# Optimization experiments

Measured on AMD Instinct MI355X. Metric: run time of the kernel, lower is better.

The kernel has to match this reference:

```python
import jax, jax.numpy as jnp
import numpy as np

QLEN, BSZ, D_MODEL = 2048, 2, 1024
N_HEAD, D_HEAD = 16, 64
SCALE = 1.0 / (D_HEAD ** 0.5)
LN_EPS = 1e-5


def _rel_shift(x):
    # x: [qlen, klen, bsz, n_head]
    q, k, b, n = x.shape
    zero_pad = jnp.zeros((q, 1, b, n), dtype=x.dtype)
    x_padded = jnp.concatenate([zero_pad, x], axis=1).reshape(k + 1, q, b, n)
    return x_padded[1:].reshape(q, k, b, n)


def setup_inputs() -> dict:
    key = jax.random.key(0)
    ks = jax.random.split(key, 6)
    w = jax.random.normal(ks[0], (QLEN, BSZ, D_MODEL), dtype=jnp.float32)
    r_emb = jax.random.normal(ks[1], (QLEN, N_HEAD, D_HEAD), dtype=jnp.float32) * 0.02
    r_w_bias = jax.random.normal(ks[2], (N_HEAD, D_HEAD), dtype=jnp.float32) * 0.02
    r_bias = jax.random.normal(ks[3], (QLEN, N_HEAD), dtype=jnp.float32) * 0.02
    # causal mask (1 above diagonal => masked), dim==2 branch of original forward
    attn_mask = jnp.triu(jnp.ones((QLEN, QLEN), dtype=jnp.float32), k=1)
    W_qkv = jax.random.normal(ks[4], (D_MODEL, 3 * N_HEAD * D_HEAD), dtype=jnp.float32) * (D_MODEL ** -0.5)
    W_o = jax.random.normal(ks[5], (N_HEAD * D_HEAD, D_MODEL), dtype=jnp.float32) * (D_MODEL ** -0.5)
    ln_g = jnp.ones((D_MODEL,), dtype=jnp.float32)
    ln_b = jnp.zeros((D_MODEL,), dtype=jnp.float32)
    return {"w": w, "r_emb": r_emb, "r_w_bias": r_w_bias, "r_bias": r_bias,
            "attn_mask": attn_mask, "W_qkv": W_qkv, "W_o": W_o, "ln_g": ln_g, "ln_b": ln_b}


def reference(w, r_emb, r_w_bias, r_bias, attn_mask, W_qkv, W_o, ln_g, ln_b):
    qlen, bsz, d_model = w.shape
    n_head, d_head = r_w_bias.shape

    w_heads = w @ W_qkv                                   # [q, b, 3*n*d]
    q_h, k_h, v_h = jnp.split(w_heads, 3, axis=-1)
    q_h = q_h.reshape(qlen, bsz, n_head, d_head)
    k_h = k_h.reshape(qlen, bsz, n_head, d_head)
    v_h = v_h.reshape(qlen, bsz, n_head, d_head)
    klen = k_h.shape[0]

    # klen == r_emb.size(0) here, so slicing is a no-op (kept for fidelity)
    r_emb_s = r_emb[-klen:]
    r_bias_s = r_bias[-klen:]

    rw_head_q = q_h + r_w_bias[None, None]                # [q, b, n, d]
    AC = jnp.einsum('ibnd,jbnd->ijbn', rw_head_q, k_h)    # content-content
    B_ = jnp.einsum('ibnd,jnd->ijbn', q_h, r_emb_s)       # content-position
    D_ = r_bias_s[None, :, None, :]                       # [1, k, 1, n]
    BD = _rel_shift(B_ + D_)

    attn_score = (AC + BD) * SCALE
    attn_score = attn_score + attn_mask[:, :, None, None] * (-1e9)
    attn_prob = jax.nn.softmax(attn_score, axis=1)

    attn_vec = jnp.einsum('ijbn,jbnd->ibnd', attn_prob, v_h)
    attn_vec = attn_vec.reshape(qlen, bsz, n_head * d_head)
    attn_out = attn_vec @ W_o

    # residual + LayerNorm
    y = w + attn_out
    mu = jnp.mean(y, axis=-1, keepdims=True)
    var = jnp.var(y, axis=-1, keepdims=True)
    return (y - mu) / jnp.sqrt(var + LN_EPS) * ln_g + ln_b
```

## Files before the change

kernel.cpp:

```cpp
#include <hip/hip_runtime.h>

typedef unsigned short ushort_t;
typedef unsigned short us4 __attribute__((ext_vector_type(4)));
typedef unsigned short us8 __attribute__((ext_vector_type(8)));
typedef unsigned int   u32x4 __attribute__((ext_vector_type(4)));
typedef float          f32x4 __attribute__((ext_vector_type(4)));
typedef __bf16         bf16x8 __attribute__((ext_vector_type(8)));

__device__ __forceinline__ unsigned short f2bf(float f) {
  unsigned u = __builtin_bit_cast(unsigned, f);
  u += 0x7fffu + ((u >> 16) & 1u);
  return (unsigned short)(u >> 16);
}
__device__ __forceinline__ float bf2f(unsigned short h) {
  unsigned u = ((unsigned)h) << 16;
  return __builtin_bit_cast(float, u);
}


__global__ __launch_bounds__(256) void k_conv_x(const float* __restrict__ in,
                                                ushort_t* __restrict__ out) {
  int i = (blockIdx.x * 256 + threadIdx.x) * 4;
  float4 v = *(const float4*)(in + i);
  us4 o;
  o[0] = f2bf(v.x); o[1] = f2bf(v.y); o[2] = f2bf(v.z); o[3] = f2bf(v.w);
  *(us4*)(out + i) = o;
}

__global__ __launch_bounds__(256) void k_transpose_bf16(const float* __restrict__ in,
                                                        ushort_t* __restrict__ out,
                                                        int R, int C) {
  __shared__ float tile[32][33];
  int c0 = blockIdx.x * 32, r0 = blockIdx.y * 32;
  int tx = threadIdx.x, ty = threadIdx.y;
#pragma unroll
  for (int k = 0; k < 32; k += 8)
    tile[ty + k][tx] = in[(size_t)(r0 + ty + k) * C + c0 + tx];
  __syncthreads();
#pragma unroll
  for (int k = 0; k < 32; k += 8)
    out[(size_t)(c0 + ty + k) * R + r0 + tx] = f2bf(tile[tx][ty + k]);
}

__global__ __launch_bounds__(256) void k_conv_remb(const float* __restrict__ re,
                                                   ushort_t* __restrict__ out) {
  int tid = blockIdx.x * 256 + threadIdx.x;
  int o = tid * 8;
  int d = o & 63, r = (o >> 6) & 2047, h = o >> 17;
  const float* src = re + ((size_t)r * 16 + h) * 64 + d;
  float4 a = *(const float4*)(src);
  float4 b = *(const float4*)(src + 4);
  us8 u;
  u[0] = f2bf(a.x); u[1] = f2bf(a.y); u[2] = f2bf(a.z); u[3] = f2bf(a.w);
  u[4] = f2bf(b.x); u[5] = f2bf(b.y); u[6] = f2bf(b.z); u[7] = f2bf(b.w);
  *(us8*)(out + o) = u;
}

__global__ __launch_bounds__(256) void k_rbias2(const ushort_t* __restrict__ RE,
                                                const float* __restrict__ rwb,
                                                const float* __restrict__ rbias,
                                                float* __restrict__ out) {
  int tid = blockIdx.x * 256 + threadIdx.x;
  int h = tid >> 11, r = tid & 2047;
  const ushort_t* re = RE + ((size_t)h * 2048 + r) * 64;
  const float* wv = rwb + h * 64;
  float acc = 0.f;
#pragma unroll
  for (int d0 = 0; d0 < 64; d0 += 8) {
    us8 v = *(const us8*)(re + d0);
#pragma unroll
    for (int e = 0; e < 8; ++e) acc += bf2f(v[e]) * wv[d0 + e];
  }
  out[h * 2048 + r] = (rbias[r * 16 + h] - acc) * 0.125f;
}


__global__ __launch_bounds__(256) void k_gemm_qkv(const ushort_t* __restrict__ A,
                                                  const ushort_t* __restrict__ B,
                                                  const float* __restrict__ rwb,
                                                  ushort_t* __restrict__ qt,
                                                  ushort_t* __restrict__ kk,
                                                  ushort_t* __restrict__ vv) {
  __shared__ ushort_t Al[128 * 32], Bl[128 * 32];
  int row0 = blockIdx.x * 128, col0 = blockIdx.y * 128;
  int t = threadIdx.x, w = t >> 6, l = t & 63;
  int wr = w >> 1, wc = w & 1, g = l >> 4, cl = l & 15;
  f32x4 acc[4][4];
#pragma unroll
  for (int m = 0; m < 4; ++m)
#pragma unroll
    for (int n = 0; n < 4; ++n) acc[m][n] = (f32x4){0.f, 0.f, 0.f, 0.f};
  for (int k0 = 0; k0 < 1024; k0 += 32) {
#pragma unroll
    for (int c = 0; c < 2; ++c) {
      int u = t + 256 * c, row = u >> 2, col = (u & 3) * 8;
      *(u32x4*)(&Al[row * 32 + col]) = *(const u32x4*)(A + (size_t)(row0 + row) * 1024 + k0 + col);
      *(u32x4*)(&Bl[row * 32 + col]) = *(const u32x4*)(B + (size_t)(col0 + row) * 1024 + k0 + col);
    }
    __syncthreads();
    bf16x8 af[4], bfr[4];
#pragma unroll
    for (int m = 0; m < 4; ++m) af[m] = *(const bf16x8*)(&Al[(wr * 64 + m * 16 + cl) * 32 + g * 8]);
#pragma unroll
    for (int n = 0; n < 4; ++n) bfr[n] = *(const bf16x8*)(&Bl[(wc * 64 + n * 16 + cl) * 32 + g * 8]);
#pragma unroll
    for (int m = 0; m < 4; ++m)
#pragma unroll
      for (int n = 0; n < 4; ++n)
        acc[m][n] = __builtin_amdgcn_mfma_f32_16x16x32_bf16(af[m], bfr[n], acc[m][n], 0, 0, 0);
    __syncthreads();
  }
  int sec = col0 >> 10;
#pragma unroll
  for (int m = 0; m < 4; ++m) {
#pragma unroll
    for (int n = 0; n < 4; ++n) {
#pragma unroll
      for (int r = 0; r < 4; ++r) {
        int row = row0 + wr * 64 + m * 16 + g * 4 + r;
        int col = col0 + wc * 64 + n * 16 + cl;
        int mm = col & 1023, hh = mm >> 6, d = mm & 63;
        int bq = row & 1, iq = row >> 1;
        float val = acc[m][n][r];
        if (sec == 0) {
          qt[(((size_t)bq * 16 + hh) * 2048 + iq) * 64 + d] = f2bf((val + rwb[mm]) * 0.125f);
        } else if (sec == 1) {
          kk[(((size_t)bq * 16 + hh) * 2048 + iq) * 64 + d] = f2bf(val);
        } else {
          vv[(((size_t)bq * 16 + hh) * 64 + d) * 2048 + iq] = f2bf(val);
        }
      }
    }
  }
}


__global__ __launch_bounds__(256, 3) void k_flash(const ushort_t* __restrict__ QT,
                                                  const ushort_t* __restrict__ KK,
                                                  const ushort_t* __restrict__ VT,
                                                  const ushort_t* __restrict__ RE,
                                                  const float* __restrict__ RB2,
                                                  ushort_t* __restrict__ AV) {
  int bh = blockIdx.x, b = bh >> 4, h = bh & 15;
  int i0 = (gridDim.y - 1 - blockIdx.y) * 64;
  int t = threadIdx.x, w = t >> 6, l = t & 63, g = l >> 4, cl = l & 15;

  __shared__ ushort_t Klds[64 * 72];
  __shared__ ushort_t Vt[64 * 72];
  __shared__ ushort_t Rl[128 * 72];
  __shared__ float rb2s[128];
  __shared__ ushort_t Pls[4][16 * 72];
  __shared__ float alphal[4][16];
  __shared__ float lsuml[4][16];

  const ushort_t* qb = QT + ((size_t)(b * 16 + h)) * 2048 * 64;
  const ushort_t* kb = KK + ((size_t)(b * 16 + h)) * 2048 * 64;
  const ushort_t* vt = VT + ((size_t)(b * 16 + h)) * 64 * 2048;
  const ushort_t* rbase = RE + (size_t)h * 2048 * 64;
  const float* r2 = RB2 + h * 2048;

  int qrow = i0 + w * 16 + cl;
  bf16x8 qa0 = *(const bf16x8*)(qb + (size_t)qrow * 64 + g * 8);
  bf16x8 qa1 = *(const bf16x8*)(qb + (size_t)qrow * 64 + 32 + g * 8);

  float m_run[4], l_run[4];
  f32x4 Ot[4];
#pragma unroll
  for (int r = 0; r < 4; ++r) { m_run[r] = -1e30f; l_run[r] = 0.f; }
#pragma unroll
  for (int dt = 0; dt < 4; ++dt) Ot[dt] = (f32x4){0.f, 0.f, 0.f, 0.f};

  int nt = gridDim.y - blockIdx.y;
  int rb0f = 1984 - i0;
  int urow = t >> 3, ucol = (t & 7) * 8;

  *(u32x4*)(&Rl[((rb0f + urow) & 127) * 72 + ucol]) =
      *(const u32x4*)(rbase + (size_t)(rb0f + urow) * 64 + ucol);
  *(u32x4*)(&Rl[((rb0f + urow + 32) & 127) * 72 + ucol]) =
      *(const u32x4*)(rbase + (size_t)(rb0f + urow + 32) * 64 + ucol);
  if (t < 64) rb2s[(rb0f + t) & 127] = r2[rb0f + t];

  u32x4 kreg0, kreg1, vreg0, vreg1, rreg0, rreg1;
  float rb2reg;

  {
    int j0n = 0;
    kreg0 = *(const u32x4*)(kb + (size_t)(j0n + urow) * 64 + ucol);
    kreg1 = *(const u32x4*)(kb + (size_t)(j0n + urow + 32) * 64 + ucol);
    vreg0 = *(const u32x4*)(vt + (size_t)urow * 2048 + j0n + ucol);
    vreg1 = *(const u32x4*)(vt + (size_t)(urow + 32) * 2048 + j0n + ucol);
    int gs = rb0f + 64;
    int rr0 = gs + urow, rr1 = gs + urow + 32;
    rreg0 = (rr0 < 2048) ? *(const u32x4*)(rbase + (size_t)rr0 * 64 + ucol) : (u32x4){0u, 0u, 0u, 0u};
    rreg1 = (rr1 < 2048) ? *(const u32x4*)(rbase + (size_t)rr1 * 64 + ucol) : (u32x4){0u, 0u, 0u, 0u};
    int rrb = gs + t;
    rb2reg = (t < 64 && rrb < 2048) ? r2[rrb] : 0.f;
  }

  for (int tt = 0; tt < nt; ++tt) {
    int j0 = tt * 64;
    int rb0 = rb0f + j0;
    __syncthreads();
    {
      *(u32x4*)(&Klds[urow * 72 + ucol]) = kreg0;
      *(u32x4*)(&Klds[(urow + 32) * 72 + ucol]) = kreg1;
      *(u32x4*)(&Vt[urow * 72 + ucol]) = vreg0;
      *(u32x4*)(&Vt[(urow + 32) * 72 + ucol]) = vreg1;
      int gs = rb0 + 64;
      *(u32x4*)(&Rl[((gs + urow) & 127) * 72 + ucol]) = rreg0;
      *(u32x4*)(&Rl[((gs + urow + 32) & 127) * 72 + ucol]) = rreg1;
      if (t < 64) rb2s[(gs + t) & 127] = rb2reg;
    }
    __syncthreads();
    if (tt + 1 < nt) {
      int j0n = j0 + 64;
      kreg0 = *(const u32x4*)(kb + (size_t)(j0n + urow) * 64 + ucol);
      kreg1 = *(const u32x4*)(kb + (size_t)(j0n + urow + 32) * 64 + ucol);
      vreg0 = *(const u32x4*)(vt + (size_t)urow * 2048 + j0n + ucol);
      vreg1 = *(const u32x4*)(vt + (size_t)(urow + 32) * 2048 + j0n + ucol);
      int gs = rb0f + j0n + 64;
      int rr0 = gs + urow, rr1 = gs + urow + 32;
      rreg0 = (rr0 < 2048) ? *(const u32x4*)(rbase + (size_t)rr0 * 64 + ucol) : (u32x4){0u, 0u, 0u, 0u};
      rreg1 = (rr1 < 2048) ? *(const u32x4*)(rbase + (size_t)rr1 * 64 + ucol) : (u32x4){0u, 0u, 0u, 0u};
      int rrb = gs + t;
      rb2reg = (t < 64 && rrb < 2048) ? r2[rrb] : 0.f;
    }

    int bw0 = 48 - 16 * w;
    int rB = rb0 + bw0;
    f32x4 bwf[5];
#pragma unroll
    for (int ct = 0; ct < 5; ++ct) {
      int prow = (rB + ct * 16) & 127;
      f32x4 a = (f32x4){0.f, 0.f, 0.f, 0.f};
      bf16x8 rr0 = *(const bf16x8*)(&Rl[(prow + cl) * 72 + g * 8]);
      a = __builtin_amdgcn_mfma_f32_16x16x32_bf16(qa0, rr0, a, 0, 0, 0);
      bf16x8 rr1 = *(const bf16x8*)(&Rl[(prow + cl) * 72 + 32 + g * 8]);
      a = __builtin_amdgcn_mfma_f32_16x16x32_bf16(qa1, rr1, a, 0, 0, 0);
      float rv = rb2s[(prow + cl) & 127];
      a[0] += rv; a[1] += rv; a[2] += rv; a[3] += rv;
      bwf[ct] = a;
    }

    f32x4 S[4];
#pragma unroll
    for (int ct = 0; ct < 4; ++ct) {
      f32x4 a = (f32x4){0.f, 0.f, 0.f, 0.f};
      bf16x8 kf0 = *(const bf16x8*)(&Klds[(ct * 16 + cl) * 72 + g * 8]);
      a = __builtin_amdgcn_mfma_f32_16x16x32_bf16(qa0, kf0, a, 0, 0, 0);
      bf16x8 kf1 = *(const bf16x8*)(&Klds[(ct * 16 + cl) * 72 + 32 + g * 8]);
      a = __builtin_amdgcn_mfma_f32_16x16x32_bf16(qa1, kf1, a, 0, 0, 0);
      S[ct] = a;
    }

    int climit = i0 - j0 + 15 + 16 * w;
#pragma unroll
    for (int r = 0; r < 4; ++r) {
      int rl = g * 4 + r;
      int dlt = cl - rl + 15;
      int src = (l & 48) | (dlt & 15);
      float b0 = __shfl(bwf[0][r], src);
      float b1 = __shfl(bwf[1][r], src);
      float b2 = __shfl(bwf[2][r], src);
      float b3 = __shfl(bwf[3][r], src);
      float b4 = __shfl(bwf[4][r], src);
      if (dlt >= 16) { b0 = b1; b1 = b2; b2 = b3; b3 = b4; }
      float sv[4];
      sv[0] = (dlt      <= climit) ? S[0][r] + b0 : -1e30f;
      sv[1] = (dlt + 16 <= climit) ? S[1][r] + b1 : -1e30f;
      sv[2] = (dlt + 32 <= climit) ? S[2][r] + b2 : -1e30f;
      sv[3] = (dlt + 48 <= climit) ? S[3][r] + b3 : -1e30f;
      float rmax = fmaxf(fmaxf(sv[0], sv[1]), fmaxf(sv[2], sv[3]));
      rmax = fmaxf(rmax, __shfl_xor(rmax, 1));
      rmax = fmaxf(rmax, __shfl_xor(rmax, 2));
      rmax = fmaxf(rmax, __shfl_xor(rmax, 4));
      rmax = fmaxf(rmax, __shfl_xor(rmax, 8));
      float mn = fmaxf(m_run[r], rmax);
      float al = __expf(m_run[r] - mn);
      m_run[r] = mn;
      float rsum = 0.f;
#pragma unroll
      for (int ct = 0; ct < 4; ++ct) {
        float pv = __expf(sv[ct] - mn);
        sv[ct] = pv;
        rsum += pv;
      }
      rsum += __shfl_xor(rsum, 1);
      rsum += __shfl_xor(rsum, 2);
      rsum += __shfl_xor(rsum, 4);
      rsum += __shfl_xor(rsum, 8);
      l_run[r] = l_run[r] * al + rsum;
      if (cl == 0) alphal[w][rl] = al;
#pragma unroll
      for (int ct = 0; ct < 4; ++ct)
        Pls[w][rl * 72 + ct * 16 + cl] = f2bf(sv[ct]);
    }
    __syncthreads();

    float aq = alphal[w][cl];
    bf16x8 pb0 = *(const bf16x8*)(&Pls[w][cl * 72 + g * 8]);
    bf16x8 pb1 = *(const bf16x8*)(&Pls[w][cl * 72 + 32 + g * 8]);
#pragma unroll
    for (int dt = 0; dt < 4; ++dt) {
      f32x4 o = Ot[dt];
      o[0] *= aq; o[1] *= aq; o[2] *= aq; o[3] *= aq;
      bf16x8 va0 = *(const bf16x8*)(&Vt[(dt * 16 + cl) * 72 + g * 8]);
      o = __builtin_amdgcn_mfma_f32_16x16x32_bf16(va0, pb0, o, 0, 0, 0);
      bf16x8 va1 = *(const bf16x8*)(&Vt[(dt * 16 + cl) * 72 + 32 + g * 8]);
      o = __builtin_amdgcn_mfma_f32_16x16x32_bf16(va1, pb1, o, 0, 0, 0);
      Ot[dt] = o;
    }
  }

  if (cl == 0) {
#pragma unroll
    for (int r = 0; r < 4; ++r) lsuml[w][g * 4 + r] = l_run[r];
  }
  float inv = 1.f / lsuml[w][cl];
  int orow = (i0 + w * 16 + cl) * 2 + b;
#pragma unroll
  for (int dt = 0; dt < 4; ++dt) {
    us4 o4;
    o4[0] = f2bf(Ot[dt][0] * inv);
    o4[1] = f2bf(Ot[dt][1] * inv);
    o4[2] = f2bf(Ot[dt][2] * inv);
    o4[3] = f2bf(Ot[dt][3] * inv);
    *(us4*)(&AV[(size_t)orow * 1024 + h * 64 + dt * 16 + g * 4]) = o4;
  }
}


__global__ __launch_bounds__(256) void k_gemm_o(const ushort_t* __restrict__ A,
                                                const ushort_t* __restrict__ B,
                                                const float* __restrict__ wsrc,
                                                float* __restrict__ Y) {
  __shared__ ushort_t Al[128 * 32], Bl[128 * 32];
  int row0 = blockIdx.x * 128, col0 = blockIdx.y * 128;
  int t = threadIdx.x, w = t >> 6, l = t & 63;
  int wr = w >> 1, wc = w & 1, g = l >> 4, cl = l & 15;
  f32x4 acc[4][4];
#pragma unroll
  for (int m = 0; m < 4; ++m)
#pragma unroll
    for (int n = 0; n < 4; ++n) acc[m][n] = (f32x4){0.f, 0.f, 0.f, 0.f};
  for (int k0 = 0; k0 < 1024; k0 += 32) {
#pragma unroll
    for (int c = 0; c < 2; ++c) {
      int u = t + 256 * c, row = u >> 2, col = (u & 3) * 8;
      *(u32x4*)(&Al[row * 32 + col]) = *(const u32x4*)(A + (size_t)(row0 + row) * 1024 + k0 + col);
      *(u32x4*)(&Bl[row * 32 + col]) = *(const u32x4*)(B + (size_t)(col0 + row) * 1024 + k0 + col);
    }
    __syncthreads();
    bf16x8 af[4], bfr[4];
#pragma unroll
    for (int m = 0; m < 4; ++m) af[m] = *(const bf16x8*)(&Al[(wr * 64 + m * 16 + cl) * 32 + g * 8]);
#pragma unroll
    for (int n = 0; n < 4; ++n) bfr[n] = *(const bf16x8*)(&Bl[(wc * 64 + n * 16 + cl) * 32 + g * 8]);
#pragma unroll
    for (int m = 0; m < 4; ++m)
#pragma unroll
      for (int n = 0; n < 4; ++n)
        acc[m][n] = __builtin_amdgcn_mfma_f32_16x16x32_bf16(af[m], bfr[n], acc[m][n], 0, 0, 0);
    __syncthreads();
  }
#pragma unroll
  for (int m = 0; m < 4; ++m) {
#pragma unroll
    for (int n = 0; n < 4; ++n) {
#pragma unroll
      for (int r = 0; r < 4; ++r) {
        int row = row0 + wr * 64 + m * 16 + g * 4 + r;
        int col = col0 + wc * 64 + n * 16 + cl;
        size_t idx = (size_t)row * 1024 + col;
        Y[idx] = acc[m][n][r] + wsrc[idx];
      }
    }
  }
}


__global__ __launch_bounds__(256) void k_ln(const float* __restrict__ Y,
                                            const float* __restrict__ gg,
                                            const float* __restrict__ bb,
                                            float* __restrict__ out) {
  int row = blockIdx.x, t = threadIdx.x;
  float4 v = *(const float4*)(Y + (size_t)row * 1024 + t * 4);
  float s = v.x + v.y + v.z + v.w;
  float q = v.x * v.x + v.y * v.y + v.z * v.z + v.w * v.w;
#pragma unroll
  for (int m = 32; m >= 1; m >>= 1) {
    s += __shfl_xor(s, m);
    q += __shfl_xor(q, m);
  }
  __shared__ float ssh[4], qsh[4];
  int w = t >> 6, l = t & 63;
  if (l == 0) { ssh[w] = s; qsh[w] = q; }
  __syncthreads();
  s = ssh[0] + ssh[1] + ssh[2] + ssh[3];
  q = qsh[0] + qsh[1] + qsh[2] + qsh[3];
  float mu = s * (1.f / 1024.f);
  float var = q * (1.f / 1024.f) - mu * mu;
  float rstd = rsqrtf(var + 1e-5f);
  float4 gv = *(const float4*)(gg + t * 4);
  float4 bv = *(const float4*)(bb + t * 4);
  float4 o;
  o.x = (v.x - mu) * rstd * gv.x + bv.x;
  o.y = (v.y - mu) * rstd * gv.y + bv.y;
  o.z = (v.z - mu) * rstd * gv.z + bv.z;
  o.w = (v.w - mu) * rstd * gv.w + bv.w;
  *(float4*)(out + (size_t)row * 1024 + t * 4) = o;
}


extern "C" void kernel_launch(void* const* d_in, const int* in_sizes, int n_in,
                              void* d_out, int out_size, void* d_ws, size_t ws_size,
                              hipStream_t stream) {
  const float* w      = (const float*)d_in[0];
  const float* r_emb  = (const float*)d_in[1];
  const float* r_w_b  = (const float*)d_in[2];
  const float* r_bias = (const float*)d_in[3];
  const float* W_qkv  = (const float*)d_in[5];
  const float* W_o    = (const float*)d_in[6];
  const float* ln_g   = (const float*)d_in[7];
  const float* ln_b   = (const float*)d_in[8];
  float* out = (float*)d_out;
  char* ws = (char*)d_ws;

  ushort_t* X16  = (ushort_t*)(ws + 0);
  ushort_t* WQ16 = (ushort_t*)(ws + 8388608);
  ushort_t* WO16 = (ushort_t*)(ws + 14680064);
  ushort_t* RE16 = (ushort_t*)(ws + 16777216);
  float*    RB2  = (float*)(ws + 20971520);
  ushort_t* QT16 = (ushort_t*)(ws + 21102592);
  ushort_t* K16  = (ushort_t*)(ws + 29491200);
  ushort_t* VT16 = (ushort_t*)(ws + 37879808);
  ushort_t* AV16 = (ushort_t*)(ws + 46268416);
  float*    Y32  = (float*)(ws + 54657024);

  k_conv_x<<<4096, 256, 0, stream>>>(w, X16);
  k_transpose_bf16<<<dim3(96, 32), dim3(32, 8), 0, stream>>>(W_qkv, WQ16, 1024, 3072);
  k_transpose_bf16<<<dim3(32, 32), dim3(32, 8), 0, stream>>>(W_o, WO16, 1024, 1024);
  k_conv_remb<<<1024, 256, 0, stream>>>(r_emb, RE16);
  k_rbias2<<<128, 256, 0, stream>>>(RE16, r_w_b, r_bias, RB2);
  k_gemm_qkv<<<dim3(32, 24), 256, 0, stream>>>(X16, WQ16, r_w_b, QT16, K16, VT16);
  k_flash<<<dim3(32, 32), 256, 0, stream>>>(QT16, K16, VT16, RE16, RB2, AV16);
  k_gemm_o<<<dim3(32, 8), 256, 0, stream>>>(AV16, WO16, w, Y32);
  k_ln<<<4096, 256, 0, stream>>>(Y32, ln_g, ln_b, out);
}
```

Before: 201.2 us.

## Enlarge flash query tile to 128 rows with 8 waves; async global-to-LDS loads in GEMMs

The flash attention kernel now handles 128 query rows per block with 512 threads (8 waves), so each K/V/R tile loaded into LDS is shared by twice as many query rows. The block count halves, and the relative-position ring buffer grows to 256 rows. Separately, both GEMMs stage A/B tiles with global_load_lds direct-to-LDS copies instead of loads through registers. The cost is more LDS per block and coarser causal-imbalance granularity. The async copies rely on the LDS layout staying contiguous, which holds because row*32+col equals u*8.

```diff
diff --git a/kernel.cpp b/kernel.cpp
--- a/kernel.cpp
+++ b/kernel.cpp
@@ -15,6 +15,12 @@
 __device__ __forceinline__ float bf2f(unsigned short h) {
   unsigned u = ((unsigned)h) << 16;
   return __builtin_bit_cast(float, u);
+}
+
+__device__ __forceinline__ void async_cp16(const ushort_t* g, ushort_t* l) {
+  __builtin_amdgcn_global_load_lds(
+      (const __attribute__((address_space(1))) unsigned int*)g,
+      (__attribute__((address_space(3))) unsigned int*)l, 16, 0, 0);
 }
 
 
@@ -94,8 +100,8 @@
 #pragma unroll
     for (int c = 0; c < 2; ++c) {
       int u = t + 256 * c, row = u >> 2, col = (u & 3) * 8;
-      *(u32x4*)(&Al[row * 32 + col]) = *(const u32x4*)(A + (size_t)(row0 + row) * 1024 + k0 + col);
-      *(u32x4*)(&Bl[row * 32 + col]) = *(const u32x4*)(B + (size_t)(col0 + row) * 1024 + k0 + col);
+      async_cp16(A + (size_t)(row0 + row) * 1024 + k0 + col, &Al[u * 8]);
+      async_cp16(B + (size_t)(col0 + row) * 1024 + k0 + col, &Bl[u * 8]);
     }
     __syncthreads();
     bf16x8 af[4], bfr[4];
@@ -135,23 +141,24 @@
 }
 
 
-__global__ __launch_bounds__(256, 3) void k_flash(const ushort_t* __restrict__ QT,
+__global__ __launch_bounds__(512, 4) void k_flash(const ushort_t* __restrict__ QT,
                                                   const ushort_t* __restrict__ KK,
                                                   const ushort_t* __restrict__ VT,
                                                   const ushort_t* __restrict__ RE,
                                                   const float* __restrict__ RB2,
                                                   ushort_t* __restrict__ AV) {
   int bh = blockIdx.x, b = bh >> 4, h = bh & 15;
-  int i0 = (gridDim.y - 1 - blockIdx.y) * 64;
+  int i0 = (gridDim.y - 1 - blockIdx.y) * 128;
   int t = threadIdx.x, w = t >> 6, l = t & 63, g = l >> 4, cl = l & 15;
+  int ib = i0 + 16 * w;
 
   __shared__ ushort_t Klds[64 * 72];
   __shared__ ushort_t Vt[64 * 72];
-  __shared__ ushort_t Rl[128 * 72];
-  __shared__ float rb2s[128];
-  __shared__ ushort_t Pls[4][16 * 72];
-  __shared__ float alphal[4][16];
-  __shared__ float lsuml[4][16];
+  __shared__ ushort_t Rl[256 * 72];
+  __shared__ float rb2s[256];
+  __shared__ ushort_t Pls[8][16 * 72];
+  __shared__ float alphal[8][16];
+  __shared__ float lsuml[8][16];
 
   const ushort_t* qb = QT + ((size_t)(b * 16 + h)) * 2048 * 64;
   const ushort_t* kb = KK + ((size_t)(b * 16 + h)) * 2048 * 64;
@@ -159,7 +166,7 @@
   const ushort_t* rbase = RE + (size_t)h * 2048 * 64;
   const float* r2 = RB2 + h * 2048;
 
-  int qrow = i0 + w * 16 + cl;
+  int qrow = ib + cl;
   bf16x8 qa0 = *(const bf16x8*)(qb + (size_t)qrow * 64 + g * 8);
   bf16x8 qa1 = *(const bf16x8*)(qb + (size_t)qrow * 64 + 32 + g * 8);
 
@@ -170,74 +177,62 @@
 #pragma unroll
   for (int dt = 0; dt < 4; ++dt) Ot[dt] = (f32x4){0.f, 0.f, 0.f, 0.f};
 
-  int nt = gridDim.y - blockIdx.y;
-  int rb0f = 1984 - i0;
+  int nt = (i0 >> 6) + 2;
+  int wbase = 1920 - i0;
   int urow = t >> 3, ucol = (t & 7) * 8;
 
-  *(u32x4*)(&Rl[((rb0f + urow) & 127) * 72 + ucol]) =
-      *(const u32x4*)(rbase + (size_t)(rb0f + urow) * 64 + ucol);
-  *(u32x4*)(&Rl[((rb0f + urow + 32) & 127) * 72 + ucol]) =
-      *(const u32x4*)(rbase + (size_t)(rb0f + urow + 32) * 64 + ucol);
-  if (t < 64) rb2s[(rb0f + t) & 127] = r2[rb0f + t];
-
-  u32x4 kreg0, kreg1, vreg0, vreg1, rreg0, rreg1;
+#pragma unroll
+  for (int c = 0; c < 2; ++c) {
+    int rr = wbase + urow + 64 * c;
+    *(u32x4*)(&Rl[(rr & 255) * 72 + ucol]) = *(const u32x4*)(rbase + (size_t)rr * 64 + ucol);
+  }
+  if (t < 128) { int rr = wbase + t; rb2s[rr & 255] = r2[rr]; }
+
+  u32x4 kreg, vreg, rreg;
   float rb2reg;
 
   {
-    int j0n = 0;
-    kreg0 = *(const u32x4*)(kb + (size_t)(j0n + urow) * 64 + ucol);
-    kreg1 = *(const u32x4*)(kb + (size_t)(j0n + urow + 32) * 64 + ucol);
-    vreg0 = *(const u32x4*)(vt + (size_t)urow * 2048 + j0n + ucol);
-    vreg1 = *(const u32x4*)(vt + (size_t)(urow + 32) * 2048 + j0n + ucol);
-    int gs = rb0f + 64;
-    int rr0 = gs + urow, rr1 = gs + urow + 32;
-    rreg0 = (rr0 < 2048) ? *(const u32x4*)(rbase + (size_t)rr0 * 64 + ucol) : (u32x4){0u, 0u, 0u, 0u};
-    rreg1 = (rr1 < 2048) ? *(const u32x4*)(rbase + (size_t)rr1 * 64 + ucol) : (u32x4){0u, 0u, 0u, 0u};
-    int rrb = gs + t;
+    kreg = *(const u32x4*)(kb + (size_t)urow * 64 + ucol);
+    vreg = *(const u32x4*)(vt + (size_t)urow * 2048 + ucol);
+    int rr = wbase + 128 + urow;
+    rreg = (rr < 2048) ? *(const u32x4*)(rbase + (size_t)rr * 64 + ucol) : (u32x4){0u, 0u, 0u, 0u};
+    int rrb = wbase + 128 + t;
     rb2reg = (t < 64 && rrb < 2048) ? r2[rrb] : 0.f;
   }
 
   for (int tt = 0; tt < nt; ++tt) {
     int j0 = tt * 64;
-    int rb0 = rb0f + j0;
     __syncthreads();
     {
-      *(u32x4*)(&Klds[urow * 72 + ucol]) = kreg0;
-      *(u32x4*)(&Klds[(urow + 32) * 72 + ucol]) = kreg1;
-      *(u32x4*)(&Vt[urow * 72 + ucol]) = vreg0;
-      *(u32x4*)(&Vt[(urow + 32) * 72 + ucol]) = vreg1;
-      int gs = rb0 + 64;
-      *(u32x4*)(&Rl[((gs + urow) & 127) * 72 + ucol]) = rreg0;
-      *(u32x4*)(&Rl[((gs + urow + 32) & 127) * 72 + ucol]) = rreg1;
-      if (t < 64) rb2s[(gs + t) & 127] = rb2reg;
+      *(u32x4*)(&Klds[urow * 72 + ucol]) = kreg;
+      *(u32x4*)(&Vt[urow * 72 + ucol]) = vreg;
+      int gs = wbase + 128 + j0;
+      *(u32x4*)(&Rl[((gs + urow) & 255) * 72 + ucol]) = rreg;
+      if (t < 64) rb2s[(gs + t) & 255] = rb2reg;
     }
     __syncthreads();
     if (tt + 1 < nt) {
       int j0n = j0 + 64;
-      kreg0 = *(const u32x4*)(kb + (size_t)(j0n + urow) * 64 + ucol);
-      kreg1 = *(const u32x4*)(kb + (size_t)(j0n + urow + 32) * 64 + ucol);
-      vreg0 = *(const u32x4*)(vt + (size_t)urow * 2048 + j0n + ucol);
-      vreg1 = *(const u32x4*)(vt + (size_t)(urow + 32) * 2048 + j0n + ucol);
-      int gs = rb0f + j0n + 64;
-      int rr0 = gs + urow, rr1 = gs + urow + 32;
-      rreg0 = (rr0 < 2048) ? *(const u32x4*)(rbase + (size_t)rr0 * 64 + ucol) : (u32x4){0u, 0u, 0u, 0u};
-      rreg1 = (rr1 < 2048) ? *(const u32x4*)(rbase + (size_t)rr1 * 64 + ucol) : (u32x4){0u, 0u, 0u, 0u};
+      kreg = *(const u32x4*)(kb + (size_t)(j0n + urow) * 64 + ucol);
+      vreg = *(const u32x4*)(vt + (size_t)(urow)*2048 + j0n + ucol);
+      int gs = wbase + 128 + j0n;
+      int rr = gs + urow;
+      rreg = (rr < 2048) ? *(const u32x4*)(rbase + (size_t)rr * 64 + ucol) : (u32x4){0u, 0u, 0u, 0u};
       int rrb = gs + t;
       rb2reg = (t < 64 && rrb < 2048) ? r2[rrb] : 0.f;
     }
 
-    int bw0 = 48 - 16 * w;
-    int rB = rb0 + bw0;
+    int rB = j0 - ib + 2032;
     f32x4 bwf[5];
 #pragma unroll
     for (int ct = 0; ct < 5; ++ct) {
-      int prow = (rB + ct * 16) & 127;
+      int prow = (rB + ct * 16) & 255;
       f32x4 a = (f32x4){0.f, 0.f, 0.f, 0.f};
       bf16x8 rr0 = *(const bf16x8*)(&Rl[(prow + cl) * 72 + g * 8]);
       a = __builtin_amdgcn_mfma_f32_16x16x32_bf16(qa0, rr0, a, 0, 0, 0);
       bf16x8 rr1 = *(const bf16x8*)(&Rl[(prow + cl) * 72 + 32 + g * 8]);
       a = __builtin_amdgcn_mfma_f32_16x16x32_bf16(qa1, rr1, a, 0, 0, 0);
-      float rv = rb2s[(prow + cl) & 127];
+      float rv = rb2s[(prow + cl) & 255];
       a[0] += rv; a[1] += rv; a[2] += rv; a[3] += rv;
       bwf[ct] = a;
     }
@@ -253,7 +248,7 @@
       S[ct] = a;
     }
 
-    int climit = i0 - j0 + 15 + 16 * w;
+    int climit = ib - j0 + 15;
 #pragma unroll
     for (int r = 0; r < 4; ++r) {
       int rl = g * 4 + r;
@@ -317,7 +312,7 @@
     for (int r = 0; r < 4; ++r) lsuml[w][g * 4 + r] = l_run[r];
   }
   float inv = 1.f / lsuml[w][cl];
-  int orow = (i0 + w * 16 + cl) * 2 + b;
+  int orow = (ib + cl) * 2 + b;
 #pragma unroll
   for (int dt = 0; dt < 4; ++dt) {
     us4 o4;
@@ -347,8 +342,8 @@
 #pragma unroll
     for (int c = 0; c < 2; ++c) {
       int u = t + 256 * c, row = u >> 2, col = (u & 3) * 8;
-      *(u32x4*)(&Al[row * 32 + col]) = *(const u32x4*)(A + (size_t)(row0 + row) * 1024 + k0 + col);
-      *(u32x4*)(&Bl[row * 32 + col]) = *(const u32x4*)(B + (size_t)(col0 + row) * 1024 + k0 + col);
+      async_cp16(A + (size_t)(row0 + row) * 1024 + k0 + col, &Al[u * 8]);
+      async_cp16(B + (size_t)(col0 + row) * 1024 + k0 + col, &Bl[u * 8]);
     }
     __syncthreads();
     bf16x8 af[4], bfr[4];
@@ -443,7 +438,7 @@
   k_conv_remb<<<1024, 256, 0, stream>>>(r_emb, RE16);
   k_rbias2<<<128, 256, 0, stream>>>(RE16, r_w_b, r_bias, RB2);
   k_gemm_qkv<<<dim3(32, 24), 256, 0, stream>>>(X16, WQ16, r_w_b, QT16, K16, VT16);
-  k_flash<<<dim3(32, 32), 256, 0, stream>>>(QT16, K16, VT16, RE16, RB2, AV16);
+  k_flash<<<dim3(32, 16), 512, 0, stream>>>(QT16, K16, VT16, RE16, RB2, AV16);
   k_gemm_o<<<dim3(32, 8), 256, 0, stream>>>(AV16, WO16, w, Y32);
   k_ln<<<4096, 256, 0, stream>>>(Y32, ln_g, ln_b, out);
 }
```

After: 227.7 us. +13.1%, slower.
